# Optimization experiments

Measured on AMD Instinct MI355X. Metric: run time of the kernel, lower is better.

The kernel has to match this reference:

```python
import jax, jax.numpy as jnp
import numpy as np

L = 8        # path length (number of visited nodes)
N = 32768    # neighbors per node (fixed fan-out)
H = 404      # relation_dim == GRU hidden size
D = 128      # node_encode_dim
F = 532      # neighbor feature = D + H
SCALE = 0.05


def setup_inputs() -> dict:
    key = jax.random.key(0)
    ks = jax.random.split(key, 14)
    return {
        "query": jax.random.normal(ks[0], (1, H), jnp.float32),
        "path_nodes": jax.random.normal(ks[1], (L, D), jnp.float32),
        "neighbors": jax.random.normal(ks[2], (L, N, F), jnp.float32),
        "action_ids": jax.random.randint(ks[3], (L - 1,), 0, N),
        "W_ih": jax.random.normal(ks[4], (3 * H, 3 * D), jnp.float32) * SCALE,
        "W_hh": jax.random.normal(ks[5], (3 * H, H), jnp.float32) * SCALE,
        "b_ih": jax.random.normal(ks[6], (3 * H,), jnp.float32) * SCALE,
        "b_hh": jax.random.normal(ks[7], (3 * H,), jnp.float32) * SCALE,
        "W_fa": jax.random.normal(ks[8], (D, F), jnp.float32) * SCALE,
        "b_fa": jax.random.normal(ks[9], (D,), jnp.float32) * SCALE,
        "W_fs": jax.random.normal(ks[10], (D, H), jnp.float32) * SCALE,
        "b_fs": jax.random.normal(ks[11], (D,), jnp.float32) * SCALE,
        "W_fp": jax.random.normal(ks[12], (1, 2 * D), jnp.float32) * SCALE,
        "b_fp": jax.random.normal(ks[13], (1,), jnp.float32) * SCALE,
    }


def gru_cell(x, h, W_ih, W_hh, b_ih, b_hh):
    # torch.nn.GRUCell semantics; x: (1, 3D), h: (1, H)
    gi = x @ W_ih.T + b_ih   # (1, 3H)
    gh = h @ W_hh.T + b_hh   # (1, 3H)
    i_r, i_z, i_n = jnp.split(gi, 3, axis=-1)
    h_r, h_z, h_n = jnp.split(gh, 3, axis=-1)
    r = jax.nn.sigmoid(i_r + h_r)
    z = jax.nn.sigmoid(i_z + h_z)
    n = jnp.tanh(i_n + r * h_n)
    return (1.0 - z) * n + z * h


def reference(query, path_nodes, neighbors, action_ids,
              W_ih, W_hh, b_ih, b_hh, W_fa, b_fa, W_fs, b_fs, W_fp, b_fp):
    # FA over all hops' neighbor blocks at once: (L, N, F) x (D, F) -> (L, N, D)
    hnts = jnp.einsum('lnf,df->lnd', neighbors, W_fa) + b_fa
    hmax = jnp.max(hnts, axis=1)                        # (L, D)  column-wise max (== _Max)
    hsel = hnts[jnp.arange(L - 1), action_ids]          # (L-1, D) chosen-action rows

    # initial GRU step: cat(zeros, zeros, first node emb) with query as hidden
    x0 = jnp.concatenate([jnp.zeros((1, 2 * D), query.dtype), path_nodes[0:1]], axis=1)
    qt = gru_cell(x0, query, W_ih, W_hh, b_ih, b_hh)

    def step(qt, inp):
        hAt, hat, nxt = inp                             # each (D,)
        x = jnp.concatenate([hAt, hat, nxt])[None, :]   # (1, 3D)
        return gru_cell(x, qt, W_ih, W_hh, b_ih, b_hh), None

    qt, _ = jax.lax.scan(step, qt, (hmax[:-1], hsel, path_nodes[1:]))

    hSt = qt @ W_fs.T + b_fs                            # (1, D)
    u0 = jnp.concatenate([hSt, hmax[-1:]], axis=1) @ W_fp.T + b_fp   # (1, 1)
    uks = hSt @ hnts[-1].T                              # (1, N)
    return jax.nn.softmax(jnp.concatenate([u0, uks], axis=1), axis=1)
```

## Files before the change

### kernel.cpp

```cpp
#include <hip/hip_runtime.h>
#include <math.h>

#define L 8
#define N 32768
#define H 404
#define D 128
#define F 532
#define KT 9
#define GRU_BLOCKS 101

typedef __attribute__((ext_vector_type(8))) _Float16 half8;
typedef __attribute__((ext_vector_type(4))) float f32x4;
typedef __attribute__((address_space(3))) unsigned int as3_u32;
typedef __attribute__((address_space(1))) unsigned int as1_u32;

#define WS_WH2     0
#define WS_HMAXK   (WS_WH2 + 36864)
#define WS_HSEL    (WS_HMAXK + L * D)
#define WS_GI      (WS_HSEL + (L - 1) * D)
#define WS_HBUF    (WS_GI + L * 3 * H)
#define WS_V       (WS_HBUF + 2 * H)
#define WS_HS      (WS_V + F)
#define WS_SCAL    (WS_HS + D)
#define WS_CNT     (WS_SCAL + 4)
#define WS_LOGITS  (WS_CNT + 4)

__device__ __forceinline__ unsigned encf(float f) {
    unsigned u = __float_as_uint(f);
    return (u & 0x80000000u) ? ~u : (u | 0x80000000u);
}
__device__ __forceinline__ float decf(unsigned u) {
    unsigned b = (u & 0x80000000u) ? (u ^ 0x80000000u) : ~u;
    return __uint_as_float(b);
}
__device__ __forceinline__ float sigmoidf_(float x) {
    return 1.0f / (1.0f + __expf(-x));
}
__device__ __forceinline__ unsigned pk_f16(float a, float b) {
    auto h = __builtin_amdgcn_cvt_pkrtz(a, b);
    return *(unsigned*)&h;
}
__device__ __forceinline__ half8 pack8(float4 x0, float4 x1) {
    uint4 u = { pk_f16(x0.x, x0.y), pk_f16(x0.z, x0.w),
                pk_f16(x1.x, x1.y), pk_f16(x1.z, x1.w) };
    return *(half8*)&u;
}
__device__ __forceinline__ void gld16(const void* g, void* l) {
    __builtin_amdgcn_global_load_lds((const as1_u32*)g, (as3_u32*)l, 16, 0, 0);
}

__global__ void k_prep(const float* __restrict__ Wfa, unsigned short* __restrict__ wh2,
                       unsigned* __restrict__ keys, unsigned* __restrict__ cnt) {
    int i = blockIdx.x * 256 + threadIdx.x;
    if (i < L * D) keys[i] = 0u;
    if (i == 2000) *cnt = 0u;
    if (i >= KT * 128 * 8) return;
    int kt = i / (128 * 8);
    int rem = i - kt * 128 * 8;
    int c = rem >> 3, j = rem & 7;
    int k0 = kt * 64 + (j ^ (c & 7)) * 8;
    unsigned short v[8];
#pragma unroll
    for (int e = 0; e < 8; ++e) {
        int k = k0 + e;
        float x = (k < F) ? Wfa[c * F + k] : 0.0f;
        _Float16 h = (_Float16)x;
        v[e] = *(unsigned short*)&h;
    }
    *(uint4*)(wh2 + (long)i * 8) = *(uint4*)v;
}

__global__ __launch_bounds__(256, 3)
void k_big(const float* __restrict__ nb, const unsigned short* __restrict__ wh2,
           const float* __restrict__ bfa, const int* __restrict__ aid,
           unsigned* __restrict__ hmaxk, float* __restrict__ hsel) {
    __shared__ float As[128 * 64];
    __shared__ unsigned short Bs[128 * 64];

    const int bid = blockIdx.x;
    const int l_hop = bid >> 8;
    const int row0 = (bid & 255) * 128;
    const int tid = threadIdx.x;
    const int lane = tid & 63, w = tid >> 6;
    const int wm = w >> 1, wn = w & 1;
    const int lr = lane & 15, kg = lane >> 4;

    const float* xbase = nb + ((long)l_hop * N + row0) * F;

    f32x4 acc[4][4];
    float bv[4];
#pragma unroll
    for (int n = 0; n < 4; ++n) bv[n] = bfa[wn * 64 + n * 16 + lr];
#pragma unroll
    for (int m = 0; m < 4; ++m)
#pragma unroll
        for (int n = 0; n < 4; ++n) {
            acc[m][n][0] = bv[n]; acc[m][n][1] = bv[n];
            acc[m][n][2] = bv[n]; acc[m][n][3] = bv[n];
        }

    const int srow = lane >> 4;
    const int scp  = lane & 15;

    for (int kt = 0; kt < KT; ++kt) {
        const int fc = kt * 64;
        __syncthreads();

#pragma unroll
        for (int it = 0; it < 8; ++it) {
            int rbase = it * 16 + w * 4;
            int row = rbase + srow;
            int cg = scp ^ (row & 7);
            int col0 = fc + cg * 4;
            const float* src = xbase + (long)row * F + ((col0 < F) ? col0 : 0);
            gld16(src, (char*)As + rbase * 256);
        }
#pragma unroll
        for (int it = 0; it < 4; ++it) {
            int rb = it * 32 + w * 8;
            const char* src = (const char*)wh2 + (long)kt * 16384 + rb * 128 + lane * 16;
            gld16(src, (char*)Bs + rb * 128);
        }
        __syncthreads();

#pragma unroll
        for (int ks = 0; ks < 2; ++ks) {
            half8 b[4];
#pragma unroll
            for (int n = 0; n < 4; ++n) {
                int col = wn * 64 + n * 16 + lr;
                int ch = (ks * 4 + kg) ^ (col & 7);
                b[n] = *(const half8*)((const char*)Bs + col * 128 + ch * 16);
            }
#pragma unroll
            for (int m = 0; m < 4; ++m) {
                int row = wm * 64 + m * 16 + lr;
                int c0 = ks * 8 + kg * 2;
                const char* base = (const char*)As + row * 256;
                float4 x0 = *(const float4*)(base + (((c0)     ^ (row & 7)) << 4));
                float4 x1 = *(const float4*)(base + (((c0 + 1) ^ (row & 7)) << 4));
                half8 a = pack8(x0, x1);
#pragma unroll
                for (int n = 0; n < 4; ++n)
                    acc[m][n] = __builtin_amdgcn_mfma_f32_16x16x32_f16(a, b[n], acc[m][n], 0, 0, 0);
            }
        }
    }

    __syncthreads();

    if (l_hop < L - 1) {
        int br = aid[l_hop] - row0;
        if (br >= 0 && br < 128 && (br >> 6) == wm && ((br >> 2) & 3) == kg) {
            int msel = (br >> 4) & 3, rsel = br & 3;
#pragma unroll
            for (int n = 0; n < 4; ++n) {
                float vsel = 0.f;
#pragma unroll
                for (int m = 0; m < 4; ++m)
#pragma unroll
                    for (int r = 0; r < 4; ++r)
                        if (m == msel && r == rsel) vsel = acc[m][n][r];
                hsel[l_hop * D + wn * 64 + n * 16 + lr] = vsel;
            }
        }
    }

    float cmax[4];
#pragma unroll
    for (int n = 0; n < 4; ++n) {
        float m0 = acc[0][n][0];
#pragma unroll
        for (int m = 0; m < 4; ++m)
#pragma unroll
            for (int r = 0; r < 4; ++r) m0 = fmaxf(m0, acc[m][n][r]);
        m0 = fmaxf(m0, __shfl_xor(m0, 16, 64));
        m0 = fmaxf(m0, __shfl_xor(m0, 32, 64));
        cmax[n] = m0;
    }
    float* wmaxp = (float*)As;
    if (kg == 0) {
#pragma unroll
        for (int n = 0; n < 4; ++n)
            wmaxp[wm * 128 + wn * 64 + n * 16 + lr] = cmax[n];
    }
    __syncthreads();
    if (tid < 128) {
        float mval = fmaxf(wmaxp[tid], wmaxp[128 + tid]);
        atomicMax(&hmaxk[l_hop * D + tid], encf(mval));
    }
}

__global__ void k_gi(const float* __restrict__ Wih, const float* __restrict__ bih,
                     const float* __restrict__ pn, const unsigned* __restrict__ hmaxk,
                     const float* __restrict__ hsel, float* __restrict__ gi) {
    __shared__ float xs[L][3 * D];
    const int tid = threadIdx.x;
    for (int i = tid; i < L * 3 * D; i += 256) {
        int t = i / (3 * D), k = i % (3 * D);
        float x;
        if (t == 0) {
            x = (k < 2 * D) ? 0.0f : pn[k - 2 * D];
        } else {
            if (k < D)            x = decf(hmaxk[(t - 1) * D + k]);
            else if (k < 2 * D)   x = hsel[(t - 1) * D + (k - D)];
            else                  x = pn[t * D + (k - 2 * D)];
        }
        xs[t][k] = x;
    }
    __syncthreads();

    const int lane = tid & 63;
    const int row = blockIdx.x * 4 + (tid >> 6);
    const float* wr = Wih + (long)row * 3 * D;
    float s[L];
#pragma unroll
    for (int t = 0; t < L; ++t) s[t] = 0.f;
#pragma unroll
    for (int c = 0; c < 6; ++c) {
        int k = lane + c * 64;
        float wv = wr[k];
#pragma unroll
        for (int t = 0; t < L; ++t) s[t] = fmaf(wv, xs[t][k], s[t]);
    }
#pragma unroll
    for (int t = 0; t < L; ++t)
        for (int off = 1; off < 64; off <<= 1) s[t] += __shfl_xor(s[t], off, 64);
    if (lane == 0) {
        float b = bih[row];
#pragma unroll
        for (int t = 0; t < L; ++t) gi[t * 3 * H + row] = s[t] + b;
    }
}

__global__ __launch_bounds__(256, 1)
void k_gru(const float* __restrict__ Whh, const float* __restrict__ bhh,
           const float* __restrict__ gi, const float* __restrict__ query,
           float* __restrict__ hbuf, unsigned* __restrict__ cnt) {
    const int tid = threadIdx.x;
    const int lane = tid & 63;
    const int j = blockIdx.x * 4 + (tid >> 6);

    float wr[7], wz[7], wnn[7];
#pragma unroll
    for (int c = 0; c < 7; ++c) {
        int i = lane + c * 64;
        bool ok = i < H;
        wr[c]  = ok ? Whh[(long)j * H + i]           : 0.f;
        wz[c]  = ok ? Whh[(long)(H + j) * H + i]     : 0.f;
        wnn[c] = ok ? Whh[(long)(2 * H + j) * H + i] : 0.f;
    }
    float b_r = 0.f, b_z = 0.f, b_n = 0.f;
    if (lane == 0) { b_r = bhh[j]; b_z = bhh[H + j]; b_n = bhh[2 * H + j]; }

    for (int t = 0; t < L; ++t) {
        const float* hin = (t == 0) ? query : (hbuf + ((t - 1) & 1) * H);
        float* hout = hbuf + (t & 1) * H;
        float pr = 0.f, pz = 0.f, pn2 = 0.f;
#pragma unroll
        for (int c = 0; c < 7; ++c) {
            int i = lane + c * 64;
            float hv = 0.f;
            if (i < H)
                hv = (t == 0) ? hin[i]
                              : __hip_atomic_load(hin + i, __ATOMIC_RELAXED,
                                                  __HIP_MEMORY_SCOPE_AGENT);
            pr  = fmaf(wr[c],  hv, pr);
            pz  = fmaf(wz[c],  hv, pz);
            pn2 = fmaf(wnn[c], hv, pn2);
        }
        for (int off = 1; off < 64; off <<= 1) {
            pr  += __shfl_xor(pr, off, 64);
            pz  += __shfl_xor(pz, off, 64);
            pn2 += __shfl_xor(pn2, off, 64);
        }
        if (lane == 0) {
            const float* gt = gi + t * 3 * H;
            float hprev = (t == 0) ? hin[j]
                                   : __hip_atomic_load(hin + j, __ATOMIC_RELAXED,
                                                       __HIP_MEMORY_SCOPE_AGENT);
            float r  = sigmoidf_(gt[j] + pr + b_r);
            float z  = sigmoidf_(gt[H + j] + pz + b_z);
            float nn = tanhf(gt[2 * H + j] + r * (pn2 + b_n));
            float hv = (1.0f - z) * nn + z * hprev;
            __hip_atomic_store(hout + j, hv, __ATOMIC_RELAXED,
                               __HIP_MEMORY_SCOPE_AGENT);
        }
        if (t < L - 1) {
            __syncthreads();
            if (tid == 0) {
                __hip_atomic_fetch_add(cnt, 1u, __ATOMIC_RELEASE,
                                       __HIP_MEMORY_SCOPE_AGENT);
                unsigned target = (unsigned)GRU_BLOCKS * (t + 1);
                while (__hip_atomic_load(cnt, __ATOMIC_ACQUIRE,
                                         __HIP_MEMORY_SCOPE_AGENT) < target)
                    __builtin_amdgcn_s_sleep(2);
            }
            __syncthreads();
        }
    }
}

__global__ void k_final(const float* __restrict__ qt, const float* __restrict__ Wfs,
                        const float* __restrict__ bfs, const float* __restrict__ Wfp,
                        const float* __restrict__ bfp, const float* __restrict__ bfa,
                        const float* __restrict__ Wfa, const unsigned* __restrict__ hmaxk,
                        float* __restrict__ v, float* __restrict__ scal,
                        float* __restrict__ logits) {
    __shared__ float hs[D];
    int tid = threadIdx.x, lane = tid & 63, wid = tid >> 6;
#pragma unroll
    for (int dd = 0; dd < 8; ++dd) {
        int d = wid * 8 + dd;
        float s = 0.f;
#pragma unroll
        for (int c = 0; c < 7; ++c) {
            int i = lane + c * 64;
            if (i < H) s = fmaf(qt[i], Wfs[(long)d * H + i], s);
        }
        for (int off = 1; off < 64; off <<= 1) s += __shfl_xor(s, off, 64);
        if (lane == 0) hs[d] = s + bfs[d];
    }
    __syncthreads();
    if (tid < F) {
        float s = 0.f;
#pragma unroll 16
        for (int d = 0; d < D; ++d) s = fmaf(hs[d], Wfa[(long)d * F + tid], s);
        v[tid] = s;
    } else if (tid == F) {
        float s = bfp[0];
        for (int d = 0; d < D; ++d) {
            s = fmaf(hs[d], Wfp[d], s);
            s = fmaf(decf(hmaxk[(L - 1) * D + d]), Wfp[D + d], s);
        }
        logits[0] = s;
    } else if (tid == F + 1) {
        float c2 = 0.f;
        for (int d = 0; d < D; ++d) c2 = fmaf(hs[d], bfa[d], c2);
        scal[0] = c2;
    }
}

__global__ void k_uks(const float* __restrict__ nb7, const float* __restrict__ v,
                      const float* __restrict__ scal, float* __restrict__ logits) {
    long n = (long)blockIdx.x * 4 + (threadIdx.x >> 6);
    int lane = threadIdx.x & 63;
    const float* row = nb7 + n * F;
    float s = 0.f;
    for (int f = lane; f < F; f += 64) s = fmaf(v[f], row[f], s);
    for (int off = 1; off < 64; off <<= 1) s += __shfl_xor(s, off, 64);
    if (lane == 0) logits[1 + n] = s + scal[0];
}

__global__ void k_sm12(const float* __restrict__ logits, float* __restrict__ scal) {
    __shared__ float sm[16], ss[16];
    int tid = threadIdx.x, lane = tid & 63, wid = tid >> 6;
    float m = -3.4e38f, s = 0.f;
    for (int i = tid; i <= N; i += 1024) {
        float x = logits[i];
        if (x > m) { s = s * __expf(m - x) + 1.0f; m = x; }
        else       { s += __expf(x - m); }
    }
    for (int off = 1; off < 64; off <<= 1) {
        float m2 = __shfl_xor(m, off, 64);
        float s2 = __shfl_xor(s, off, 64);
        float M = fmaxf(m, m2);
        s = s * __expf(m - M) + s2 * __expf(m2 - M);
        m = M;
    }
    if (lane == 0) { sm[wid] = m; ss[wid] = s; }
    __syncthreads();
    if (tid == 0) {
        float M = sm[0], S = 0.f;
        for (int k = 1; k < 16; ++k) M = fmaxf(M, sm[k]);
        for (int k = 0; k < 16; ++k) S += ss[k] * __expf(sm[k] - M);
        scal[1] = M; scal[2] = S;
    }
}

__global__ void k_sm3(const float* __restrict__ logits, const float* __restrict__ scal,
                      float* __restrict__ out) {
    int i = blockIdx.x * 256 + threadIdx.x;
    if (i <= N) out[i] = __expf(logits[i] - scal[1]) / scal[2];
}

extern "C" void kernel_launch(void* const* d_in, const int* in_sizes, int n_in,
                              void* d_out, int out_size, void* d_ws, size_t ws_size,
                              hipStream_t stream) {
    const float* query = (const float*)d_in[0];
    const float* pn    = (const float*)d_in[1];
    const float* nb    = (const float*)d_in[2];
    const int*   aid   = (const int*)d_in[3];
    const float* Wih   = (const float*)d_in[4];
    const float* Whh   = (const float*)d_in[5];
    const float* bih   = (const float*)d_in[6];
    const float* bhh   = (const float*)d_in[7];
    const float* Wfa   = (const float*)d_in[8];
    const float* bfa   = (const float*)d_in[9];
    const float* Wfs   = (const float*)d_in[10];
    const float* bfs   = (const float*)d_in[11];
    const float* Wfp   = (const float*)d_in[12];
    const float* bfp   = (const float*)d_in[13];

    float* ws = (float*)d_ws;
    unsigned short* wh2   = (unsigned short*)(ws + WS_WH2);
    unsigned*       hmaxk = (unsigned*)(ws + WS_HMAXK);
    unsigned*       cnt   = (unsigned*)(ws + WS_CNT);
    float* hsel   = ws + WS_HSEL;
    float* gi     = ws + WS_GI;
    float* hbuf   = ws + WS_HBUF;
    float* v      = ws + WS_V;
    float* scal   = ws + WS_SCAL;
    float* logits = ws + WS_LOGITS;
    float* out    = (float*)d_out;

    k_prep<<<(KT * 128 * 8 + 255) / 256, 256, 0, stream>>>(Wfa, wh2, hmaxk, cnt);
    k_big <<<L * 256, 256, 0, stream>>>(nb, wh2, bfa, aid, hmaxk, hsel);
    k_gi  <<<303, 256, 0, stream>>>(Wih, bih, pn, hmaxk, hsel, gi);
    k_gru <<<GRU_BLOCKS, 256, 0, stream>>>(Whh, bhh, gi, query, hbuf, cnt);

    const float* qt = hbuf + ((L - 1) & 1) * H;
    k_final<<<1, 1024, 0, stream>>>(qt, Wfs, bfs, Wfp, bfp, bfa, Wfa, hmaxk, v, scal, logits);
    k_uks  <<<N / 4, 256, 0, stream>>>(nb + (long)(L - 1) * N * F, v, scal, logits);

    k_sm12<<<1, 1024, 0, stream>>>(logits, scal);
    k_sm3 <<<(N + 1 + 255) / 256, 256, 0, stream>>>(logits, scal, out);
}
```

Measured before the change: 226.0 us.

## Fuse last-hop logits and partial softmax into a deferred hop-7 GEMM

The GEMM for the last hop now runs after the GRU as a separate template instantiation of the big MFMA kernel. Its epilogue dots each output row with hS to produce the logits directly, and writes per-block max and sum partials for the softmax. The GRU kernel now also computes hS = qt·W_fs^T + b_fs after one extra grid barrier, so the separate final kernel, the fp32 logits kernel that re-read the whole hop-7 neighbor block, and the full logits scan in the softmax kernel are all removed. The cost is that the hop-7 GEMM launches as only 256 blocks on the critical path after the GRU, which may leave the GPU under-occupied.

```diff
diff --git a/kernel.cpp b/kernel.cpp
--- a/kernel.cpp
+++ b/kernel.cpp
@@ -19,11 +19,12 @@
 #define WS_HSEL    (WS_HMAXK + L * D)
 #define WS_GI      (WS_HSEL + (L - 1) * D)
 #define WS_HBUF    (WS_GI + L * 3 * H)
-#define WS_V       (WS_HBUF + 2 * H)
-#define WS_HS      (WS_V + F)
+#define WS_HS      (WS_HBUF + 2 * H)
 #define WS_SCAL    (WS_HS + D)
 #define WS_CNT     (WS_SCAL + 4)
-#define WS_LOGITS  (WS_CNT + 4)
+#define WS_PM      (WS_CNT + 4)
+#define WS_PS      (WS_PM + 256)
+#define WS_LOGITS  (WS_PS + 256)
 
 __device__ __forceinline__ unsigned encf(float f) {
     unsigned u = __float_as_uint(f);
@@ -47,6 +48,12 @@
 }
 __device__ __forceinline__ void gld16(const void* g, void* l) {
     __builtin_amdgcn_global_load_lds((const as1_u32*)g, (as3_u32*)l, 16, 0, 0);
+}
+__device__ __forceinline__ float aload(const float* p) {
+    return __hip_atomic_load(p, __ATOMIC_RELAXED, __HIP_MEMORY_SCOPE_AGENT);
+}
+__device__ __forceinline__ void astore(float* p, float v) {
+    __hip_atomic_store(p, v, __ATOMIC_RELAXED, __HIP_MEMORY_SCOPE_AGENT);
 }
 
 __global__ void k_prep(const float* __restrict__ Wfa, unsigned short* __restrict__ wh2,
@@ -70,16 +77,20 @@
     *(uint4*)(wh2 + (long)i * 8) = *(uint4*)v;
 }
 
+template<int HOP7>
 __global__ __launch_bounds__(256, 3)
 void k_big(const float* __restrict__ nb, const unsigned short* __restrict__ wh2,
            const float* __restrict__ bfa, const int* __restrict__ aid,
-           unsigned* __restrict__ hmaxk, float* __restrict__ hsel) {
+           unsigned* __restrict__ hmaxk, float* __restrict__ hsel,
+           const float* __restrict__ hs_ws, float* __restrict__ logits,
+           float* __restrict__ pm, float* __restrict__ ps) {
     __shared__ float As[128 * 64];
     __shared__ unsigned short Bs[128 * 64];
+    __shared__ float sm2[2], ss2[2];
 
     const int bid = blockIdx.x;
-    const int l_hop = bid >> 8;
-    const int row0 = (bid & 255) * 128;
+    const int l_hop = HOP7 ? 7 : (bid >> 8);
+    const int row0 = HOP7 ? bid * 128 : (bid & 255) * 128;
     const int tid = threadIdx.x;
     const int lane = tid & 63, w = tid >> 6;
     const int wm = w >> 1, wn = w & 1;
@@ -105,7 +116,6 @@
     for (int kt = 0; kt < KT; ++kt) {
         const int fc = kt * 64;
         __syncthreads();
-
 #pragma unroll
         for (int it = 0; it < 8; ++it) {
             int rbase = it * 16 + w * 4;
@@ -149,7 +159,7 @@
 
     __syncthreads();
 
-    if (l_hop < L - 1) {
+    if (!HOP7) {
         int br = aid[l_hop] - row0;
         if (br >= 0 && br < 128 && (br >> 6) == wm && ((br >> 2) & 3) == kg) {
             int msel = (br >> 4) & 3, rsel = br & 3;
@@ -164,6 +174,55 @@
                 hsel[l_hop * D + wn * 64 + n * 16 + lr] = vsel;
             }
         }
+    } else {
+        float hsv[4];
+#pragma unroll
+        for (int n = 0; n < 4; ++n) hsv[n] = hs_ws[wn * 64 + n * 16 + lr];
+        float p[4][4];
+#pragma unroll
+        for (int m = 0; m < 4; ++m)
+#pragma unroll
+            for (int r = 0; r < 4; ++r) {
+                float s = hsv[0] * acc[m][0][r];
+                s = fmaf(hsv[1], acc[m][1][r], s);
+                s = fmaf(hsv[2], acc[m][2][r], s);
+                s = fmaf(hsv[3], acc[m][3][r], s);
+#pragma unroll
+                for (int off = 1; off < 16; off <<= 1)
+                    s += __shfl_xor(s, off, 64);
+                p[m][r] = s;
+            }
+        float* part = (float*)As;
+        if (lr == 0) {
+#pragma unroll
+            for (int m = 0; m < 4; ++m)
+#pragma unroll
+                for (int r = 0; r < 4; ++r)
+                    part[wn * 128 + wm * 64 + m * 16 + kg * 4 + r] = p[m][r];
+        }
+        __syncthreads();
+        float val = -3.4e38f, sv = 0.f;
+        if (tid < 128) {
+            val = part[tid] + part[128 + tid];
+            logits[1 + row0 + tid] = val;
+            sv = 1.0f;
+        }
+        float mv = val;
+        for (int off = 1; off < 64; off <<= 1) {
+            float m2 = __shfl_xor(mv, off, 64);
+            float s2 = __shfl_xor(sv, off, 64);
+            float M = fmaxf(mv, m2);
+            sv = sv * __expf(mv - M) + s2 * __expf(m2 - M);
+            mv = M;
+        }
+        if (lane == 0 && w < 2) { sm2[w] = mv; ss2[w] = sv; }
+        __syncthreads();
+        if (tid == 0) {
+            float M = fmaxf(sm2[0], sm2[1]);
+            float S = ss2[0] * __expf(sm2[0] - M) + ss2[1] * __expf(sm2[1] - M);
+            pm[bid] = M; ps[bid] = S;
+        }
+        __syncthreads();
     }
 
     float cmax[4];
@@ -236,10 +295,13 @@
 __global__ __launch_bounds__(256, 1)
 void k_gru(const float* __restrict__ Whh, const float* __restrict__ bhh,
            const float* __restrict__ gi, const float* __restrict__ query,
-           float* __restrict__ hbuf, unsigned* __restrict__ cnt) {
+           const float* __restrict__ Wfs, const float* __restrict__ bfs,
+           float* __restrict__ hbuf, float* __restrict__ hs_ws,
+           unsigned* __restrict__ cnt) {
     const int tid = threadIdx.x;
     const int lane = tid & 63;
-    const int j = blockIdx.x * 4 + (tid >> 6);
+    const int bid = blockIdx.x;
+    const int j = bid * 4 + (tid >> 6);
 
     float wr[7], wz[7], wnn[7];
 #pragma unroll
@@ -261,10 +323,7 @@
         for (int c = 0; c < 7; ++c) {
             int i = lane + c * 64;
             float hv = 0.f;
-            if (i < H)
-                hv = (t == 0) ? hin[i]
-                              : __hip_atomic_load(hin + i, __ATOMIC_RELAXED,
-                                                  __HIP_MEMORY_SCOPE_AGENT);
+            if (i < H) hv = (t == 0) ? hin[i] : aload(hin + i);
             pr  = fmaf(wr[c],  hv, pr);
             pz  = fmaf(wz[c],  hv, pz);
             pn2 = fmaf(wnn[c], hv, pn2);
@@ -276,91 +335,55 @@
         }
         if (lane == 0) {
             const float* gt = gi + t * 3 * H;
-            float hprev = (t == 0) ? hin[j]
-                                   : __hip_atomic_load(hin + j, __ATOMIC_RELAXED,
-                                                       __HIP_MEMORY_SCOPE_AGENT);
+            float hprev = (t == 0) ? hin[j] : aload(hin + j);
             float r  = sigmoidf_(gt[j] + pr + b_r);
             float z  = sigmoidf_(gt[H + j] + pz + b_z);
             float nn = tanhf(gt[2 * H + j] + r * (pn2 + b_n));
-            float hv = (1.0f - z) * nn + z * hprev;
-            __hip_atomic_store(hout + j, hv, __ATOMIC_RELAXED,
-                               __HIP_MEMORY_SCOPE_AGENT);
-        }
-        if (t < L - 1) {
-            __syncthreads();
-            if (tid == 0) {
-                __hip_atomic_fetch_add(cnt, 1u, __ATOMIC_RELEASE,
-                                       __HIP_MEMORY_SCOPE_AGENT);
-                unsigned target = (unsigned)GRU_BLOCKS * (t + 1);
-                while (__hip_atomic_load(cnt, __ATOMIC_ACQUIRE,
-                                         __HIP_MEMORY_SCOPE_AGENT) < target)
-                    __builtin_amdgcn_s_sleep(2);
-            }
-            __syncthreads();
-        }
-    }
-}
-
-__global__ void k_final(const float* __restrict__ qt, const float* __restrict__ Wfs,
-                        const float* __restrict__ bfs, const float* __restrict__ Wfp,
-                        const float* __restrict__ bfp, const float* __restrict__ bfa,
-                        const float* __restrict__ Wfa, const unsigned* __restrict__ hmaxk,
-                        float* __restrict__ v, float* __restrict__ scal,
-                        float* __restrict__ logits) {
-    __shared__ float hs[D];
-    int tid = threadIdx.x, lane = tid & 63, wid = tid >> 6;
-#pragma unroll
-    for (int dd = 0; dd < 8; ++dd) {
-        int d = wid * 8 + dd;
+            astore(hout + j, (1.0f - z) * nn + z * hprev);
+        }
+        __syncthreads();
+        if (tid == 0) {
+            __hip_atomic_fetch_add(cnt, 1u, __ATOMIC_RELEASE,
+                                   __HIP_MEMORY_SCOPE_AGENT);
+            unsigned target = (unsigned)GRU_BLOCKS * (t + 1);
+            while (__hip_atomic_load(cnt, __ATOMIC_ACQUIRE,
+                                     __HIP_MEMORY_SCOPE_AGENT) < target)
+                __builtin_amdgcn_s_sleep(2);
+        }
+        __syncthreads();
+    }
+
+    if (bid < 32) {
+        const float* qt = hbuf + H;
+        int d = bid * 4 + (tid >> 6);
         float s = 0.f;
 #pragma unroll
         for (int c = 0; c < 7; ++c) {
             int i = lane + c * 64;
-            if (i < H) s = fmaf(qt[i], Wfs[(long)d * H + i], s);
+            if (i < H) s = fmaf(aload(qt + i), Wfs[(long)d * H + i], s);
         }
         for (int off = 1; off < 64; off <<= 1) s += __shfl_xor(s, off, 64);
-        if (lane == 0) hs[d] = s + bfs[d];
+        if (lane == 0) astore(&hs_ws[d], s + bfs[d]);
+    }
+}
+
+__global__ void k_sm12(const float* __restrict__ hs_ws, const float* __restrict__ Wfp,
+                       const float* __restrict__ bfp, const unsigned* __restrict__ hmaxk,
+                       const float* __restrict__ pm, const float* __restrict__ ps,
+                       float* __restrict__ logits, float* __restrict__ scal) {
+    __shared__ float red[4], reds[4], u0sh;
+    int tid = threadIdx.x, lane = tid & 63, wid = tid >> 6;
+    if (tid < 64) {
+        float s = hs_ws[tid] * Wfp[tid];
+        s = fmaf(hs_ws[tid + 64], Wfp[tid + 64], s);
+        s = fmaf(decf(hmaxk[(L - 1) * D + tid]),      Wfp[D + tid],      s);
+        s = fmaf(decf(hmaxk[(L - 1) * D + tid + 64]), Wfp[D + tid + 64], s);
+        for (int off = 1; off < 64; off <<= 1) s += __shfl_xor(s, off, 64);
+        if (tid == 0) { u0sh = s + bfp[0]; logits[0] = u0sh; }
     }
     __syncthreads();
-    if (tid < F) {
-        float s = 0.f;
-#pragma unroll 16
-        for (int d = 0; d < D; ++d) s = fmaf(hs[d], Wfa[(long)d * F + tid], s);
-        v[tid] = s;
-    } else if (tid == F) {
-        float s = bfp[0];
-        for (int d = 0; d < D; ++d) {
-            s = fmaf(hs[d], Wfp[d], s);
-            s = fmaf(decf(hmaxk[(L - 1) * D + d]), Wfp[D + d], s);
-        }
-        logits[0] = s;
-    } else if (tid == F + 1) {
-        float c2 = 0.f;
-        for (int d = 0; d < D; ++d) c2 = fmaf(hs[d], bfa[d], c2);
-        scal[0] = c2;
-    }
-}
-
-__global__ void k_uks(const float* __restrict__ nb7, const float* __restrict__ v,
-                      const float* __restrict__ scal, float* __restrict__ logits) {
-    long n = (long)blockIdx.x * 4 + (threadIdx.x >> 6);
-    int lane = threadIdx.x & 63;
-    const float* row = nb7 + n * F;
-    float s = 0.f;
-    for (int f = lane; f < F; f += 64) s = fmaf(v[f], row[f], s);
-    for (int off = 1; off < 64; off <<= 1) s += __shfl_xor(s, off, 64);
-    if (lane == 0) logits[1 + n] = s + scal[0];
-}
-
-__global__ void k_sm12(const float* __restrict__ logits, float* __restrict__ scal) {
-    __shared__ float sm[16], ss[16];
-    int tid = threadIdx.x, lane = tid & 63, wid = tid >> 6;
     float m = -3.4e38f, s = 0.f;
-    for (int i = tid; i <= N; i += 1024) {
-        float x = logits[i];
-        if (x > m) { s = s * __expf(m - x) + 1.0f; m = x; }
-        else       { s += __expf(x - m); }
-    }
+    if (tid < 256) { m = pm[tid]; s = ps[tid]; }
     for (int off = 1; off < 64; off <<= 1) {
         float m2 = __shfl_xor(m, off, 64);
         float s2 = __shfl_xor(s, off, 64);
@@ -368,12 +391,15 @@
         s = s * __expf(m - M) + s2 * __expf(m2 - M);
         m = M;
     }
-    if (lane == 0) { sm[wid] = m; ss[wid] = s; }
+    if (lane == 0 && wid < 4) { red[wid] = m; reds[wid] = s; }
     __syncthreads();
     if (tid == 0) {
-        float M = sm[0], S = 0.f;
-        for (int k = 1; k < 16; ++k) M = fmaxf(M, sm[k]);
-        for (int k = 0; k < 16; ++k) S += ss[k] * __expf(sm[k] - M);
+        float M = u0sh, S = 1.0f;
+        for (int k = 0; k < 4; ++k) {
+            float Mn = fmaxf(M, red[k]);
+            S = S * __expf(M - Mn) + reds[k] * __expf(red[k] - Mn);
+            M = Mn;
+        }
         scal[1] = M; scal[2] = S;
     }
 }
@@ -409,20 +435,21 @@
     float* hsel   = ws + WS_HSEL;
     float* gi     = ws + WS_GI;
     float* hbuf   = ws + WS_HBUF;
-    float* v      = ws + WS_V;
+    float* hs_ws  = ws + WS_HS;
     float* scal   = ws + WS_SCAL;
+    float* pm     = ws + WS_PM;
+    float* psum   = ws + WS_PS;
     float* logits = ws + WS_LOGITS;
     float* out    = (float*)d_out;
 
     k_prep<<<(KT * 128 * 8 + 255) / 256, 256, 0, stream>>>(Wfa, wh2, hmaxk, cnt);
-    k_big <<<L * 256, 256, 0, stream>>>(nb, wh2, bfa, aid, hmaxk, hsel);
+    k_big<0><<<(L - 1) * 256, 256, 0, stream>>>(nb, wh2, bfa, aid, hmaxk, hsel,
+                                                hs_ws, logits, pm, psum);
     k_gi  <<<303, 256, 0, stream>>>(Wih, bih, pn, hmaxk, hsel, gi);
-    k_gru <<<GRU_BLOCKS, 256, 0, stream>>>(Whh, bhh, gi, query, hbuf, cnt);
-
-    const float* qt = hbuf + ((L - 1) & 1) * H;
-    k_final<<<1, 1024, 0, stream>>>(qt, Wfs, bfs, Wfp, bfp, bfa, Wfa, hmaxk, v, scal, logits);
-    k_uks  <<<N / 4, 256, 0, stream>>>(nb + (long)(L - 1) * N * F, v, scal, logits);
-
-    k_sm12<<<1, 1024, 0, stream>>>(logits, scal);
+    k_gru <<<GRU_BLOCKS, 256, 0, stream>>>(Whh, bhh, gi, query, Wfs, bfs,
+                                           hbuf, hs_ws, cnt);
+    k_big<1><<<256, 256, 0, stream>>>(nb, wh2, bfa, aid, hmaxk, hsel,
+                                      hs_ws, logits, pm, psum);
+    k_sm12<<<1, 1024, 0, stream>>>(hs_ws, Wfp, bfp, hmaxk, pm, psum, logits, scal);
     k_sm3 <<<(N + 1 + 255) / 256, 256, 0, stream>>>(logits, scal, out);
 }
```

Measured after the change: 195.1 us. -13.7%, faster.
